# Kernel tuning notes

Hardware: AMD Instinct MI355X
Metric: run time of the kernel (lower is better)

## Reference

```python
import jax, jax.numpy as jnp
from jax import lax
import numpy as np

B, D, P, C = 16384, 256, 512, 20  # batch, input_dim, prototype_dim, n_class


def setup_inputs() -> dict:
    key = jax.random.key(0)
    k1, k2, k3 = jax.random.split(key, 3)
    return {
        "inputs": jax.random.normal(k1, (B, D), dtype=jnp.float32),
        "W": jax.random.normal(k2, (P, D), dtype=jnp.float32),
        "BETA": jax.random.normal(k3, (P, C), dtype=jnp.float32),
        "alpha": jnp.zeros((P, 1), dtype=jnp.float32),
        "gamma": jnp.full((P, 1), 0.1, dtype=jnp.float32),
        "n_class": C,
        "prototype_dim": P,
    }


def reference(inputs, W, BETA, alpha, gamma, n_class, prototype_dim):
    # inputs: [B, D], W: [P, D], BETA: [P, C], alpha/gamma: [P, 1]
    BETA2 = BETA * BETA
    U = BETA2 / BETA2.sum(axis=1, keepdims=True)          # [P, C]
    alphap = 0.99 / (1.0 + jnp.exp(-alpha))               # [P, 1]
    # d[k, b] = 0.5 * ||x_b - W_k||^2 via the expanded quadratic form
    d = 0.5 * (jnp.sum(W * W, axis=1)[:, None]
               + jnp.sum(inputs * inputs, axis=1)[None, :]
               - 2.0 * W @ inputs.T)                      # [P, B]
    expo = jnp.exp(-(gamma * gamma) * d)                  # [P, B]
    s = alphap * expo                                     # [P, B]

    bsz = inputs.shape[0]

    def step(mk, xs):
        # mk: [C+1, B] combined mass; xs = (U_k [C], s_k [B])
        Uk, sk = xs
        m_c = Uk[:, None] * sk[None, :]                   # [C, B] singleton masses
        m_n = 1.0 - sk                                    # [B]   mass on ignorance
        mk_c, mk_n = mk[:-1], mk[-1]
        new_c = mk_c * (m_c + m_n[None, :]) + m_c * mk_n[None, :]
        new_n = mk_n * m_n
        return jnp.concatenate([new_c, new_n[None, :]], axis=0), None

    mk0 = jnp.concatenate([jnp.zeros((n_class, bsz), dtype=inputs.dtype),
                           jnp.ones((1, bsz), dtype=inputs.dtype)], axis=0)
    mk, _ = lax.scan(step, mk0, (U, s))                   # sequential over P prototypes
    K = mk.sum(axis=0)                                    # [B]
    return (mk / K[None, :]).T                            # [B, C+1]
```

## Files before the change

kernel.cpp:

```cpp
#include <hip/hip_runtime.h>
#include <math.h>


#define NBATCH 16384
#define ND     256
#define NP     512
#define NCLS   20
#define OC     21

typedef short  short8  __attribute__((ext_vector_type(8)));
typedef short  short4v __attribute__((ext_vector_type(4)));
typedef unsigned short ushort8 __attribute__((ext_vector_type(8)));
typedef float  f32x16  __attribute__((ext_vector_type(16)));

#define OFF_PWH 0u
#define OFF_PWL 262144u
#define OFF_VS  524288u
#define OFF_WQ  567296u
#define OFF_AP  569344u
#define OFF_G2  571392u
#define OFF_PP  1048576u
#define WS_BIG  ((size_t)(OFF_PP + 2752512u))

__device__ __forceinline__ unsigned short f2bf_rn(float f) {
  unsigned int u = __float_as_uint(f);
  unsigned int r = (u + 0x7FFFu + ((u >> 16) & 1u)) >> 16;
  return (unsigned short)r;
}
__device__ __forceinline__ float bf2f(unsigned short h) {
  return __uint_as_float(((unsigned int)h) << 16);
}

__global__ __launch_bounds__(256)
void prep(const float* __restrict__ Wsrc, const float* __restrict__ BETA,
          const float* __restrict__ alpha, const float* __restrict__ gamma,
          unsigned short* __restrict__ dh, unsigned short* __restrict__ dl,
          float* __restrict__ sq, float* __restrict__ VS,
          float* __restrict__ AP, float* __restrict__ G2)
{
  const int bid = blockIdx.x;
  if (bid < 64) {
    const int tid = bid * 256 + threadIdx.x;
    const int row = tid >> 5, seg = tid & 31;
    const float4* s4 = (const float4*)(Wsrc + (size_t)row * ND + seg * 8);
    const float4 a = s4[0], b = s4[1];
    const float v[8] = {a.x, a.y, a.z, a.w, b.x, b.y, b.z, b.w};
    ushort8 hv, lv;
    float ssq = 0.f;
    #pragma unroll
    for (int j = 0; j < 8; ++j) {
      ssq = fmaf(v[j], v[j], ssq);
      const unsigned short hh = f2bf_rn(v[j]);
      hv[j] = hh;
      lv[j] = f2bf_rn(v[j] - bf2f(hh));
    }
    const int tile = row >> 5, m = row & 31, step = seg >> 1, r = seg & 1;
    const size_t cidx = (size_t)(tile * 16 + step) * 64 + m + 32 * r;
    *(ushort8*)(dh + cidx * 8) = hv;
    *(ushort8*)(dl + cidx * 8) = lv;
    #pragma unroll
    for (int off = 1; off < 32; off <<= 1) ssq += __shfl_xor(ssq, off, 64);
    if (seg == 0) sq[row] = ssq;
  } else {
    const int k = (bid - 64) * 256 + threadIdx.x;
    if (k >= NP) return;
    float bv[NCLS], bs = 0.f;
    #pragma unroll
    for (int c = 0; c < NCLS; ++c) { bv[c] = BETA[k * NCLS + c]; bs = fmaf(bv[c], bv[c], bs); }
    const float binv = 1.f / bs;
    #pragma unroll
    for (int c = 0; c < NCLS; ++c) VS[c * NP + k] = 1.f - bv[c] * bv[c] * binv;
    VS[NCLS * NP + k] = 1.f;
    AP[k] = 0.99f / (1.f + __expf(-alpha[k]));
    const float g = gamma[k];
    G2[k] = g * g;
  }
}

__device__ __forceinline__ void mfma_pass(
    const short* __restrict__ Ah, const short* __restrict__ Al,
    const short8* __restrict__ bHc, const short8* __restrict__ bLc,
    const int lane, const int sh, const float* __restrict__ xqs,
    const float wqk, const float apk, const float g2k, float* __restrict__ sout)
{
  short8 wbh[4], wbl[4];
  #pragma unroll
  for (int p = 0; p < 4; ++p) { wbh[p] = bHc[p * 64]; wbl[p] = bLc[p * 64]; }

  f32x16 accA, accB;
  #pragma unroll
  for (int i = 0; i < 16; ++i) { accA[i] = 0.f; accB[i] = 0.f; }
  const short8* aH = (const short8*)Ah + (size_t)sh * 1024 + lane;
  const short8* aL = (const short8*)Al + (size_t)sh * 1024 + lane;
  #pragma unroll
  for (int step = 0; step < 16; ++step) {
    const short8 ah = aH[step * 64], al = aL[step * 64];
    const short8 bh = wbh[step & 3], bl = wbl[step & 3];
    if (step < 12) {
      wbh[step & 3] = bHc[(step + 4) * 64];
      wbl[step & 3] = bLc[(step + 4) * 64];
    }
    accA = __builtin_amdgcn_mfma_f32_32x32x16_bf16(ah, bh, accA, 0, 0, 0);
    accB = __builtin_amdgcn_mfma_f32_32x32x16_bf16(ah, bl, accB, 0, 0, 0);
    accB = __builtin_amdgcn_mfma_f32_32x32x16_bf16(al, bh, accB, 0, 0, 0);
  }
  const int h = lane >> 5;
  #pragma unroll
  for (int rg = 0; rg < 16; ++rg) {
    const int   m  = (rg & 3) + 8 * (rg >> 2) + 4 * h;
    const float dv = 0.5f * (wqk + xqs[sh * 32 + m]) - (accA[rg] + accB[rg]);
    sout[rg] = apk * __expf(-g2k * dv);
  }
}

__global__ __launch_bounds__(512)
void gemm_comb(const float* __restrict__ X,
               const unsigned short* __restrict__ PWH, const unsigned short* __restrict__ PWL,
               const float* __restrict__ VS, const float* __restrict__ WQ,
               const float* __restrict__ AP, const float* __restrict__ G2,
               float* __restrict__ PP)
{
  __shared__ __align__(16) char pool[65536];
  __shared__ float xqs[64];
  short* Ah = (short*)pool;
  short* Al = (short*)(pool + 32768);
  float* sc = (float*)pool;

  const int t    = threadIdx.x;
  const int lane = t & 63;
  const int wv   = __builtin_amdgcn_readfirstlane(t >> 6);
  const int bx   = blockIdx.x;
  const int tile = bx >> 1, half = bx & 1;
  const int bbase = tile * 64;
  const int pl = lane & 31, h = lane >> 5;

  {
    const int r  = t >> 3;
    const int sg = t & 7;
    const int rsh = r >> 5, rm = r & 31;
    const float* xrow = X + (size_t)(bbase + r) * ND;
    float ssq = 0.f;
    #pragma unroll
    for (int it = 0; it < 8; ++it) {
      const int c0 = it * 32 + sg * 4;
      const float4 v = *(const float4*)(xrow + c0);
      const float vv[4] = {v.x, v.y, v.z, v.w};
      short4v h4, l4;
      #pragma unroll
      for (int j = 0; j < 4; ++j) {
        ssq = fmaf(vv[j], vv[j], ssq);
        const unsigned short hh = f2bf_rn(vv[j]);
        h4[j] = (short)hh;
        l4[j] = (short)f2bf_rn(vv[j] - bf2f(hh));
      }
      const int step = c0 >> 4, hf = (c0 >> 3) & 1, j0 = c0 & 7;
      const int base = (((rsh * 16 + step) * 64) + (rm + 32 * hf)) * 8 + j0;
      *(short4v*)&Ah[base] = h4;
      *(short4v*)&Al[base] = l4;
    }
    ssq += __shfl_xor(ssq, 1, 64);
    ssq += __shfl_xor(ssq, 2, 64);
    ssq += __shfl_xor(ssq, 4, 64);
    if (sg == 0) xqs[r] = ssq;
  }
  __syncthreads();

  const int kp = half * 256 + wv * 32 + pl;
  const float wqk = WQ[kp], apk = AP[kp], g2k = G2[kp];
  const short8* bHc = (const short8*)PWH + (size_t)(half * 8 + wv) * 1024 + lane;
  const short8* bLc = (const short8*)PWL + (size_t)(half * 8 + wv) * 1024 + lane;

  float sreg0[16], sreg1[16];
  mfma_pass(Ah, Al, bHc, bLc, lane, 0, xqs, wqk, apk, g2k, sreg0);
  mfma_pass(Ah, Al, bHc, bLc, lane, 1, xqs, wqk, apk, g2k, sreg1);

  __syncthreads();

  {
    const int p = wv * 32 + pl;
    #pragma unroll
    for (int rg = 0; rg < 16; ++rg) {
      const int m  = (rg & 3) + 8 * (rg >> 2) + 4 * h;
      sc[m * 256 + ((p + 4 * m) & 255)] = sreg0[rg];
      const int b1 = m + 32;
      sc[b1 * 256 + ((p + 4 * b1) & 255)] = sreg1[rg];
    }
  }
  __syncthreads();

  float Apc[OC];
  {
    const int j3 = wv;
    float sv[32];
    const int c0 = (j3 * 32 + 4 * lane);
    #pragma unroll
    for (int q = 0; q < 8; ++q)
      *(float4*)&sv[4 * q] = *(const float4*)&sc[lane * 256 + ((c0 + 4 * q) & 255)];

    const float* vt = VS + half * 256 + j3 * 32;
    for (int c = 0; c < OC; ++c) {
      const float* vp = vt + (size_t)c * NP;
      float f8[8];
      #pragma unroll
      for (int j = 0; j < 8; ++j) f8[j] = fmaf(-sv[j], vp[j], 1.0f);
      #pragma unroll
      for (int j = 8; j < 32; ++j) f8[j & 7] *= fmaf(-sv[j], vp[j], 1.0f);
      Apc[c] = ((f8[0] * f8[1]) * (f8[2] * f8[3])) *
               ((f8[4] * f8[5]) * (f8[6] * f8[7]));
    }
  }
  __syncthreads();

  float* E = (float*)pool;
  #pragma unroll
  for (int c = 0; c < OC; ++c) E[(wv * OC + c) * 64 + lane] = Apc[c];
  __syncthreads();
  {
    const int b = t & 63, j = t >> 6;
    float* pp = PP + (size_t)bx * (OC * 64);
    for (int c = j; c < OC; c += 8) {
      float p = E[c * 64 + b];
      #pragma unroll
      for (int w = 1; w < 8; ++w) p *= E[(w * OC + c) * 64 + b];
      pp[c * 64 + b] = p;
    }
  }
}

__global__ __launch_bounds__(256)
void finish(const float* __restrict__ PP, float* __restrict__ OUT)
{
  const int s = blockIdx.x * 256 + threadIdx.x;
  const int tile = s >> 6, b = s & 63;
  const float* p0 = PP + (size_t)tile * (2 * OC * 64) + b;
  const float* p1 = p0 + OC * 64;
  float A[OC];
  #pragma unroll
  for (int c = 0; c < OC; ++c) A[c] = p0[c * 64] * p1[c * 64];
  const float Nv = A[NCLS];
  float K = Nv;
  #pragma unroll
  for (int c = 0; c < NCLS; ++c) K += A[c] - Nv;
  const float ik = 1.0f / K;
  float* o = OUT + (size_t)s * OC;
  #pragma unroll
  for (int c = 0; c < NCLS; ++c) o[c] = (A[c] - Nv) * ik;
  o[NCLS] = Nv * ik;
}

__global__ __launch_bounds__(512)
void evid_main(const float* __restrict__ X,
               const unsigned short* __restrict__ PWH, const unsigned short* __restrict__ PWL,
               const float* __restrict__ VS, const float* __restrict__ WQ,
               const float* __restrict__ AP, const float* __restrict__ G2,
               float* __restrict__ OUT)
{
  __shared__ __align__(16) short Ah[16384], Al[16384];
  __shared__ __align__(16) float sst[2][8192];
  __shared__ float xqs[64];

  const int t    = threadIdx.x;
  const int lane = t & 63;
  const int wv   = __builtin_amdgcn_readfirstlane(t >> 6);
  const int tile = blockIdx.x;
  const int bbase = tile * 64;
  const int sh = wv & 1, pg = wv >> 1;
  const int pl = lane & 31, h = lane >> 5;

  const short8* bH = (const short8*)PWH + (size_t)pg * 1024 + lane;
  const short8* bL = (const short8*)PWL + (size_t)pg * 1024 + lane;
  short8 wbh[4], wbl[4];
  #pragma unroll
  for (int p = 0; p < 4; ++p) { wbh[p] = bH[p * 64]; wbl[p] = bL[p * 64]; }

  {
    const int r  = t >> 3;
    const int sg = t & 7;
    const int rsh = r >> 5, rm = r & 31;
    const float* xrow = X + (size_t)(bbase + r) * ND;
    float ssq = 0.f;
    #pragma unroll
    for (int it = 0; it < 8; ++it) {
      const int c0 = it * 32 + sg * 4;
      const float4 v = *(const float4*)(xrow + c0);
      const float vv[4] = {v.x, v.y, v.z, v.w};
      short4v h4, l4;
      #pragma unroll
      for (int j = 0; j < 4; ++j) {
        ssq = fmaf(vv[j], vv[j], ssq);
        const unsigned short hh = f2bf_rn(vv[j]);
        h4[j] = (short)hh;
        l4[j] = (short)f2bf_rn(vv[j] - bf2f(hh));
      }
      const int step = c0 >> 4, hf = (c0 >> 3) & 1, j0 = c0 & 7;
      const int base = (((rsh * 16 + step) * 64) + (rm + 32 * hf)) * 8 + j0;
      *(short4v*)&Ah[base] = h4;
      *(short4v*)&Al[base] = l4;
    }
    ssq += __shfl_xor(ssq, 1, 64);
    ssq += __shfl_xor(ssq, 2, 64);
    ssq += __shfl_xor(ssq, 4, 64);
    if (sg == 0) xqs[r] = ssq;
  }
  __syncthreads();

  float xqv[16];
  #pragma unroll
  for (int rg = 0; rg < 16; ++rg)
    xqv[rg] = xqs[sh * 32 + (rg & 3) + 8 * (rg >> 2) + 4 * h];

  float Apc[OC];
  #pragma unroll
  for (int c = 0; c < OC; ++c) Apc[c] = 1.0f;

  #pragma unroll 1
  for (int chunk = 0; chunk < 4; ++chunk) {
    const int par = chunk & 1;
    float* sp = &sst[par][0];
    const int kp = chunk * 128 + pg * 32 + pl;
    const float wqk = WQ[kp], apk = AP[kp], g2k = G2[kp];

    f32x16 accA, accB, accC;
    #pragma unroll
    for (int i = 0; i < 16; ++i) { accA[i] = 0.f; accB[i] = 0.f; accC[i] = 0.f; }
    const short8* aH = (const short8*)Ah + (size_t)sh * 1024 + lane;
    const short8* aL = (const short8*)Al + (size_t)sh * 1024 + lane;
    #pragma unroll
    for (int step = 0; step < 16; ++step) {
      const short8 ah = aH[step * 64], al = aL[step * 64];
      const short8 bh = wbh[step & 3], bl = wbl[step & 3];
      if (step < 12) {
        wbh[step & 3] = bH[(step + 4) * 64];
        wbl[step & 3] = bL[(step + 4) * 64];
      }
      accA = __builtin_amdgcn_mfma_f32_32x32x16_bf16(ah, bh, accA, 0, 0, 0);
      accB = __builtin_amdgcn_mfma_f32_32x32x16_bf16(ah, bl, accB, 0, 0, 0);
      accC = __builtin_amdgcn_mfma_f32_32x32x16_bf16(al, bh, accC, 0, 0, 0);
    }

    #pragma unroll
    for (int rg = 0; rg < 16; ++rg) {
      const int   m  = (rg & 3) + 8 * (rg >> 2) + 4 * h;
      const int   b  = sh * 32 + m;
      const int   col = (pg * 32 + pl + 4 * m) & 127;
      const float dv = 0.5f * (wqk + xqv[rg]) - (accA[rg] + accB[rg] + accC[rg]);
      sp[b * 128 + col] = apk * __expf(-g2k * dv);
    }

    if (chunk < 3) {
      bH += 4096; bL += 4096;
      #pragma unroll
      for (int p = 0; p < 4; ++p) { wbh[p] = bH[p * 64]; wbl[p] = bL[p * 64]; }
    }

    __syncthreads();

    {
      const int kl = wv * 16;
      float sv[16];
      #pragma unroll
      for (int q = 0; q < 4; ++q) {
        const int col = (kl + 4 * (lane & 31) + 4 * q) & 127;
        *(float4*)&sv[4 * q] = *(const float4*)&sp[lane * 128 + col];
      }
      const float* vtab = VS + chunk * 128 + kl;
      for (int c = 0; c < OC; ++c) {
        const float* vp = vtab + (size_t)c * NP;
        float f[16];
        #pragma unroll
        for (int j = 0; j < 16; ++j) f[j] = fmaf(-sv[j], vp[j], 1.0f);
        const float p0 = (f[0] * f[1]) * (f[2] * f[3]);
        const float p1 = (f[4] * f[5]) * (f[6] * f[7]);
        const float p2 = (f[8] * f[9]) * (f[10] * f[11]);
        const float p3 = (f[12] * f[13]) * (f[14] * f[15]);
        Apc[c] *= (p0 * p1) * (p2 * p3);
      }
    }
  }

  __syncthreads();
  float* S = &sst[0][0];
  #pragma unroll
  for (int c = 0; c < OC; ++c) S[(wv * OC + c) * 64 + lane] = Apc[c];
  __syncthreads();
  float* R  = S + 11008;
  {
    const int b = t & 63, j = t >> 6;
    for (int c = j; c < OC; c += 8) {
      float p = S[c * 64 + b];
      #pragma unroll
      for (int w = 1; w < 8; ++w) p *= S[(w * OC + c) * 64 + b];
      R[c * 64 + b] = p;
    }
  }
  __syncthreads();
  float* kv = R + 1344;
  if (t < 64) {
    const float Nv = R[NCLS * 64 + t];
    float K = Nv;
    #pragma unroll
    for (int c = 0; c < NCLS; ++c) K += R[c * 64 + t] - Nv;
    kv[t] = 1.0f / K;
  }
  __syncthreads();
  for (int idx = t; idx < 64 * OC; idx += 512) {
    const int b = idx / OC, c = idx - b * OC;
    const float Nv = R[NCLS * 64 + b];
    const float ik = kv[b];
    OUT[(size_t)tile * 64 * OC + idx] = (c < NCLS) ? (R[c * 64 + b] - Nv) * ik : Nv * ik;
  }
}

extern "C" void kernel_launch(void* const* d_in, const int* in_sizes, int n_in,
                              void* d_out, int out_size, void* d_ws, size_t ws_size,
                              hipStream_t stream) {
  (void)in_sizes; (void)n_in; (void)out_size;
  const float* X     = (const float*)d_in[0];
  const float* Wm    = (const float*)d_in[1];
  const float* BETA  = (const float*)d_in[2];
  const float* ALPHA = (const float*)d_in[3];
  const float* GAMMA = (const float*)d_in[4];
  float* OUT = (float*)d_out;

  char* ws = (char*)d_ws;
  unsigned short* PWH = (unsigned short*)(ws + OFF_PWH);
  unsigned short* PWL = (unsigned short*)(ws + OFF_PWL);
  float* VS = (float*)(ws + OFF_VS);
  float* WQ = (float*)(ws + OFF_WQ);
  float* AP = (float*)(ws + OFF_AP);
  float* G2 = (float*)(ws + OFF_G2);

  hipLaunchKernelGGL(prep, dim3(66), dim3(256), 0, stream,
                     Wm, BETA, ALPHA, GAMMA, PWH, PWL, WQ, VS, AP, G2);

  if (ws_size >= WS_BIG) {
    float* PP = (float*)(ws + OFF_PP);
    hipLaunchKernelGGL(gemm_comb, dim3(NBATCH/32), dim3(512), 0, stream,
                       X, PWH, PWL, VS, WQ, AP, G2, PP);
    hipLaunchKernelGGL(finish, dim3(NBATCH/256), dim3(256), 0, stream,
                       PP, OUT);
  } else {
    hipLaunchKernelGGL(evid_main, dim3(NBATCH/64), dim3(512), 0, stream,
                       X, PWH, PWL, VS, WQ, AP, G2, OUT);
  }
}
```

Before: 100.1 us.

## Fuse GEMM, combination and finish into one 1024-thread block per tile

Replaces the two-kernel path (gemm_comb writing per-half partial products to workspace, then a finish kernel) with a single 1024-thread kernel per 64-row tile. All 512 prototypes are handled in one block, and the normalization happens in-block. This removes the partial-product round trip through global memory and one launch. In exchange it uses about 128KB of LDS and 1024 threads per block, which limits occupancy to roughly one block per CU, and it serializes the two prototype halves through shared memory with extra barriers.

```diff
diff --git a/kernel.cpp b/kernel.cpp
--- a/kernel.cpp
+++ b/kernel.cpp
@@ -19,8 +19,6 @@
 #define OFF_WQ  567296u
 #define OFF_AP  569344u
 #define OFF_G2  571392u
-#define OFF_PP  1048576u
-#define WS_BIG  ((size_t)(OFF_PP + 2752512u))
 
 __device__ __forceinline__ unsigned short f2bf_rn(float f) {
   unsigned int u = __float_as_uint(f);
@@ -113,36 +111,35 @@
   }
 }
 
-__global__ __launch_bounds__(512)
-void gemm_comb(const float* __restrict__ X,
-               const unsigned short* __restrict__ PWH, const unsigned short* __restrict__ PWL,
-               const float* __restrict__ VS, const float* __restrict__ WQ,
-               const float* __restrict__ AP, const float* __restrict__ G2,
-               float* __restrict__ PP)
+__global__ __launch_bounds__(1024)
+void evid_fused(const float* __restrict__ X,
+                const unsigned short* __restrict__ PWH, const unsigned short* __restrict__ PWL,
+                const float* __restrict__ VS, const float* __restrict__ WQ,
+                const float* __restrict__ AP, const float* __restrict__ G2,
+                float* __restrict__ OUT)
 {
-  __shared__ __align__(16) char pool[65536];
-  __shared__ float xqs[64];
-  short* Ah = (short*)pool;
-  short* Al = (short*)(pool + 32768);
-  float* sc = (float*)pool;
+  __shared__ __align__(16) char pool[131328];
+  short* Ah  = (short*)pool;
+  short* Al  = (short*)(pool + 32768);
+  float* sc  = (float*)(pool + 65536);
+  float* xqs = (float*)(pool + 131072);
 
   const int t    = threadIdx.x;
   const int lane = t & 63;
-  const int wv   = __builtin_amdgcn_readfirstlane(t >> 6);
-  const int bx   = blockIdx.x;
-  const int tile = bx >> 1, half = bx & 1;
+  const int w    = __builtin_amdgcn_readfirstlane(t >> 6);
+  const int tile = blockIdx.x;
   const int bbase = tile * 64;
   const int pl = lane & 31, h = lane >> 5;
 
   {
-    const int r  = t >> 3;
-    const int sg = t & 7;
+    const int r  = t >> 4;
+    const int sg = t & 15;
     const int rsh = r >> 5, rm = r & 31;
     const float* xrow = X + (size_t)(bbase + r) * ND;
     float ssq = 0.f;
     #pragma unroll
-    for (int it = 0; it < 8; ++it) {
-      const int c0 = it * 32 + sg * 4;
+    for (int it = 0; it < 4; ++it) {
+      const int c0 = it * 64 + sg * 4;
       const float4 v = *(const float4*)(xrow + c0);
       const float vv[4] = {v.x, v.y, v.z, v.w};
       short4v h4, l4;
@@ -161,240 +158,80 @@
     ssq += __shfl_xor(ssq, 1, 64);
     ssq += __shfl_xor(ssq, 2, 64);
     ssq += __shfl_xor(ssq, 4, 64);
+    ssq += __shfl_xor(ssq, 8, 64);
     if (sg == 0) xqs[r] = ssq;
   }
   __syncthreads();
 
-  const int kp = half * 256 + wv * 32 + pl;
+  const int kp = w * 32 + pl;
   const float wqk = WQ[kp], apk = AP[kp], g2k = G2[kp];
-  const short8* bHc = (const short8*)PWH + (size_t)(half * 8 + wv) * 1024 + lane;
-  const short8* bLc = (const short8*)PWL + (size_t)(half * 8 + wv) * 1024 + lane;
+  const short8* bHc = (const short8*)PWH + (size_t)w * 1024 + lane;
+  const short8* bLc = (const short8*)PWL + (size_t)w * 1024 + lane;
 
   float sreg0[16], sreg1[16];
   mfma_pass(Ah, Al, bHc, bLc, lane, 0, xqs, wqk, apk, g2k, sreg0);
   mfma_pass(Ah, Al, bHc, bLc, lane, 1, xqs, wqk, apk, g2k, sreg1);
 
-  __syncthreads();
-
-  {
-    const int p = wv * 32 + pl;
-    #pragma unroll
-    for (int rg = 0; rg < 16; ++rg) {
-      const int m  = (rg & 3) + 8 * (rg >> 2) + 4 * h;
-      sc[m * 256 + ((p + 4 * m) & 255)] = sreg0[rg];
-      const int b1 = m + 32;
-      sc[b1 * 256 + ((p + 4 * b1) & 255)] = sreg1[rg];
-    }
-  }
-  __syncthreads();
-
   float Apc[OC];
-  {
-    const int j3 = wv;
-    float sv[32];
-    const int c0 = (j3 * 32 + 4 * lane);
-    #pragma unroll
-    for (int q = 0; q < 8; ++q)
-      *(float4*)&sv[4 * q] = *(const float4*)&sc[lane * 256 + ((c0 + 4 * q) & 255)];
-
-    const float* vt = VS + half * 256 + j3 * 32;
-    for (int c = 0; c < OC; ++c) {
-      const float* vp = vt + (size_t)c * NP;
-      float f8[8];
-      #pragma unroll
-      for (int j = 0; j < 8; ++j) f8[j] = fmaf(-sv[j], vp[j], 1.0f);
-      #pragma unroll
-      for (int j = 8; j < 32; ++j) f8[j & 7] *= fmaf(-sv[j], vp[j], 1.0f);
-      Apc[c] = ((f8[0] * f8[1]) * (f8[2] * f8[3])) *
-               ((f8[4] * f8[5]) * (f8[6] * f8[7]));
+  #pragma unroll
+  for (int c = 0; c < OC; ++c) Apc[c] = 1.0f;
+
+  const int j8 = w & 7, kh = w >> 3;
+  const int c0r = j8 * 32 + kh * 16;
+
+  #pragma unroll
+  for (int pp = 0; pp < 2; ++pp) {
+    if (pp == 1) __syncthreads();
+    if (kh == pp) {
+      const int p = j8 * 32 + pl;
+      #pragma unroll
+      for (int rg = 0; rg < 16; ++rg) {
+        const int m  = (rg & 3) + 8 * (rg >> 2) + 4 * h;
+        sc[m * 256 + ((p + 4 * m) & 255)] = sreg0[rg];
+        const int b1 = m + 32;
+        sc[b1 * 256 + ((p + 4 * b1) & 255)] = sreg1[rg];
+      }
+    }
+    __syncthreads();
+
+    {
+      float sv[16];
+      #pragma unroll
+      for (int u = 0; u < 4; ++u)
+        *(float4*)&sv[4 * u] =
+          *(const float4*)&sc[lane * 256 + ((c0r + 4 * lane + 4 * u) & 255)];
+
+      const float* vt = VS + pp * 256 + c0r;
+      for (int c = 0; c < OC; ++c) {
+        const float* vp = vt + (size_t)c * NP;
+        float f8[8];
+        #pragma unroll
+        for (int j = 0; j < 8; ++j) f8[j] = fmaf(-sv[j], vp[j], 1.0f);
+        #pragma unroll
+        for (int j = 8; j < 16; ++j) f8[j & 7] *= fmaf(-sv[j], vp[j], 1.0f);
+        Apc[c] *= ((f8[0] * f8[1]) * (f8[2] * f8[3])) *
+                  ((f8[4] * f8[5]) * (f8[6] * f8[7]));
+      }
     }
   }
   __syncthreads();
 
   float* E = (float*)pool;
   #pragma unroll
-  for (int c = 0; c < OC; ++c) E[(wv * OC + c) * 64 + lane] = Apc[c];
-  __syncthreads();
+  for (int c = 0; c < OC; ++c) E[(w * OC + c) * 64 + lane] = Apc[c];
+  __syncthreads();
+  float* R  = (float*)(pool + 88064);
+  float* kv = (float*)(pool + 93440);
   {
     const int b = t & 63, j = t >> 6;
-    float* pp = PP + (size_t)bx * (OC * 64);
-    for (int c = j; c < OC; c += 8) {
+    for (int c = j; c < OC; c += 16) {
       float p = E[c * 64 + b];
       #pragma unroll
-      for (int w = 1; w < 8; ++w) p *= E[(w * OC + c) * 64 + b];
-      pp[c * 64 + b] = p;
-    }
-  }
-}
-
-__global__ __launch_bounds__(256)
-void finish(const float* __restrict__ PP, float* __restrict__ OUT)
-{
-  const int s = blockIdx.x * 256 + threadIdx.x;
-  const int tile = s >> 6, b = s & 63;
-  const float* p0 = PP + (size_t)tile * (2 * OC * 64) + b;
-  const float* p1 = p0 + OC * 64;
-  float A[OC];
-  #pragma unroll
-  for (int c = 0; c < OC; ++c) A[c] = p0[c * 64] * p1[c * 64];
-  const float Nv = A[NCLS];
-  float K = Nv;
-  #pragma unroll
-  for (int c = 0; c < NCLS; ++c) K += A[c] - Nv;
-  const float ik = 1.0f / K;
-  float* o = OUT + (size_t)s * OC;
-  #pragma unroll
-  for (int c = 0; c < NCLS; ++c) o[c] = (A[c] - Nv) * ik;
-  o[NCLS] = Nv * ik;
-}
-
-__global__ __launch_bounds__(512)
-void evid_main(const float* __restrict__ X,
-               const unsigned short* __restrict__ PWH, const unsigned short* __restrict__ PWL,
-               const float* __restrict__ VS, const float* __restrict__ WQ,
-               const float* __restrict__ AP, const float* __restrict__ G2,
-               float* __restrict__ OUT)
-{
-  __shared__ __align__(16) short Ah[16384], Al[16384];
-  __shared__ __align__(16) float sst[2][8192];
-  __shared__ float xqs[64];
-
-  const int t    = threadIdx.x;
-  const int lane = t & 63;
-  const int wv   = __builtin_amdgcn_readfirstlane(t >> 6);
-  const int tile = blockIdx.x;
-  const int bbase = tile * 64;
-  const int sh = wv & 1, pg = wv >> 1;
-  const int pl = lane & 31, h = lane >> 5;
-
-  const short8* bH = (const short8*)PWH + (size_t)pg * 1024 + lane;
-  const short8* bL = (const short8*)PWL + (size_t)pg * 1024 + lane;
-  short8 wbh[4], wbl[4];
-  #pragma unroll
-  for (int p = 0; p < 4; ++p) { wbh[p] = bH[p * 64]; wbl[p] = bL[p * 64]; }
-
-  {
-    const int r  = t >> 3;
-    const int sg = t & 7;
-    const int rsh = r >> 5, rm = r & 31;
-    const float* xrow = X + (size_t)(bbase + r) * ND;
-    float ssq = 0.f;
-    #pragma unroll
-    for (int it = 0; it < 8; ++it) {
-      const int c0 = it * 32 + sg * 4;
-      const float4 v = *(const float4*)(xrow + c0);
-      const float vv[4] = {v.x, v.y, v.z, v.w};
-      short4v h4, l4;
-      #pragma unroll
-      for (int j = 0; j < 4; ++j) {
-        ssq = fmaf(vv[j], vv[j], ssq);
-        const unsigned short hh = f2bf_rn(vv[j]);
-        h4[j] = (short)hh;
-        l4[j] = (short)f2bf_rn(vv[j] - bf2f(hh));
-      }
-      const int step = c0 >> 4, hf = (c0 >> 3) & 1, j0 = c0 & 7;
-      const int base = (((rsh * 16 + step) * 64) + (rm + 32 * hf)) * 8 + j0;
-      *(short4v*)&Ah[base] = h4;
-      *(short4v*)&Al[base] = l4;
-    }
-    ssq += __shfl_xor(ssq, 1, 64);
-    ssq += __shfl_xor(ssq, 2, 64);
-    ssq += __shfl_xor(ssq, 4, 64);
-    if (sg == 0) xqs[r] = ssq;
-  }
-  __syncthreads();
-
-  float xqv[16];
-  #pragma unroll
-  for (int rg = 0; rg < 16; ++rg)
-    xqv[rg] = xqs[sh * 32 + (rg & 3) + 8 * (rg >> 2) + 4 * h];
-
-  float Apc[OC];
-  #pragma unroll
-  for (int c = 0; c < OC; ++c) Apc[c] = 1.0f;
-
-  #pragma unroll 1
-  for (int chunk = 0; chunk < 4; ++chunk) {
-    const int par = chunk & 1;
-    float* sp = &sst[par][0];
-    const int kp = chunk * 128 + pg * 32 + pl;
-    const float wqk = WQ[kp], apk = AP[kp], g2k = G2[kp];
-
-    f32x16 accA, accB, accC;
-    #pragma unroll
-    for (int i = 0; i < 16; ++i) { accA[i] = 0.f; accB[i] = 0.f; accC[i] = 0.f; }
-    const short8* aH = (const short8*)Ah + (size_t)sh * 1024 + lane;
-    const short8* aL = (const short8*)Al + (size_t)sh * 1024 + lane;
-    #pragma unroll
-    for (int step = 0; step < 16; ++step) {
-      const short8 ah = aH[step * 64], al = aL[step * 64];
-      const short8 bh = wbh[step & 3], bl = wbl[step & 3];
-      if (step < 12) {
-        wbh[step & 3] = bH[(step + 4) * 64];
-        wbl[step & 3] = bL[(step + 4) * 64];
-      }
-      accA = __builtin_amdgcn_mfma_f32_32x32x16_bf16(ah, bh, accA, 0, 0, 0);
-      accB = __builtin_amdgcn_mfma_f32_32x32x16_bf16(ah, bl, accB, 0, 0, 0);
-      accC = __builtin_amdgcn_mfma_f32_32x32x16_bf16(al, bh, accC, 0, 0, 0);
-    }
-
-    #pragma unroll
-    for (int rg = 0; rg < 16; ++rg) {
-      const int   m  = (rg & 3) + 8 * (rg >> 2) + 4 * h;
-      const int   b  = sh * 32 + m;
-      const int   col = (pg * 32 + pl + 4 * m) & 127;
-      const float dv = 0.5f * (wqk + xqv[rg]) - (accA[rg] + accB[rg] + accC[rg]);
-      sp[b * 128 + col] = apk * __expf(-g2k * dv);
-    }
-
-    if (chunk < 3) {
-      bH += 4096; bL += 4096;
-      #pragma unroll
-      for (int p = 0; p < 4; ++p) { wbh[p] = bH[p * 64]; wbl[p] = bL[p * 64]; }
-    }
-
-    __syncthreads();
-
-    {
-      const int kl = wv * 16;
-      float sv[16];
-      #pragma unroll
-      for (int q = 0; q < 4; ++q) {
-        const int col = (kl + 4 * (lane & 31) + 4 * q) & 127;
-        *(float4*)&sv[4 * q] = *(const float4*)&sp[lane * 128 + col];
-      }
-      const float* vtab = VS + chunk * 128 + kl;
-      for (int c = 0; c < OC; ++c) {
-        const float* vp = vtab + (size_t)c * NP;
-        float f[16];
-        #pragma unroll
-        for (int j = 0; j < 16; ++j) f[j] = fmaf(-sv[j], vp[j], 1.0f);
-        const float p0 = (f[0] * f[1]) * (f[2] * f[3]);
-        const float p1 = (f[4] * f[5]) * (f[6] * f[7]);
-        const float p2 = (f[8] * f[9]) * (f[10] * f[11]);
-        const float p3 = (f[12] * f[13]) * (f[14] * f[15]);
-        Apc[c] *= (p0 * p1) * (p2 * p3);
-      }
-    }
-  }
-
-  __syncthreads();
-  float* S = &sst[0][0];
-  #pragma unroll
-  for (int c = 0; c < OC; ++c) S[(wv * OC + c) * 64 + lane] = Apc[c];
-  __syncthreads();
-  float* R  = S + 11008;
-  {
-    const int b = t & 63, j = t >> 6;
-    for (int c = j; c < OC; c += 8) {
-      float p = S[c * 64 + b];
-      #pragma unroll
-      for (int w = 1; w < 8; ++w) p *= S[(w * OC + c) * 64 + b];
+      for (int ww = 1; ww < 16; ++ww) p *= E[(ww * OC + c) * 64 + b];
       R[c * 64 + b] = p;
     }
   }
   __syncthreads();
-  float* kv = R + 1344;
   if (t < 64) {
     const float Nv = R[NCLS * 64 + t];
     float K = Nv;
@@ -403,7 +240,7 @@
     kv[t] = 1.0f / K;
   }
   __syncthreads();
-  for (int idx = t; idx < 64 * OC; idx += 512) {
+  for (int idx = t; idx < 64 * OC; idx += 1024) {
     const int b = idx / OC, c = idx - b * OC;
     const float Nv = R[NCLS * 64 + b];
     const float ik = kv[b];
@@ -414,7 +251,7 @@
 extern "C" void kernel_launch(void* const* d_in, const int* in_sizes, int n_in,
                               void* d_out, int out_size, void* d_ws, size_t ws_size,
                               hipStream_t stream) {
-  (void)in_sizes; (void)n_in; (void)out_size;
+  (void)in_sizes; (void)n_in; (void)out_size; (void)ws_size;
   const float* X     = (const float*)d_in[0];
   const float* Wm    = (const float*)d_in[1];
   const float* BETA  = (const float*)d_in[2];
@@ -432,15 +269,6 @@
 
   hipLaunchKernelGGL(prep, dim3(66), dim3(256), 0, stream,
                      Wm, BETA, ALPHA, GAMMA, PWH, PWL, WQ, VS, AP, G2);
-
-  if (ws_size >= WS_BIG) {
-    float* PP = (float*)(ws + OFF_PP);
-    hipLaunchKernelGGL(gemm_comb, dim3(NBATCH/32), dim3(512), 0, stream,
-                       X, PWH, PWL, VS, WQ, AP, G2, PP);
-    hipLaunchKernelGGL(finish, dim3(NBATCH/256), dim3(256), 0, stream,
-                       PP, OUT);
-  } else {
-    hipLaunchKernelGGL(evid_main, dim3(NBATCH/64), dim3(512), 0, stream,
-                       X, PWH, PWL, VS, WQ, AP, G2, OUT);
-  }
-}
+  hipLaunchKernelGGL(evid_fused, dim3(NBATCH / 64), dim3(1024), 0, stream,
+                     X, PWH, PWL, VS, WQ, AP, G2, OUT);
+}
```

After: 249.6 us. 2.49x slower.
